# Performance work log

Measured on AMD Instinct MI355X. Metric: run time of the kernel, lower is better.

The kernel has to match this reference:

```python
import jax, jax.numpy as jnp
import numpy as np

B, HORIZON, F, ORDER, K = 8192, 64, 64, 16, 256


def setup_inputs() -> dict:
    key = jax.random.key(0)
    ks = jax.random.split(key, 7)
    s = 0.05
    x = jax.random.normal(ks[0], (B, HORIZON, F), dtype=jnp.float32)
    y0 = jax.random.normal(ks[1], (B, ORDER), dtype=jnp.float32)
    kernel = jax.random.normal(ks[2], (F + ORDER, 4 * K), dtype=jnp.float32) * s
    rec_kernel = jax.random.normal(ks[3], (K, 4 * K), dtype=jnp.float32) * s
    bias = jax.random.normal(ks[4], (4 * K,), dtype=jnp.float32) * s
    dense_w = jax.random.normal(ks[5], (K, 1), dtype=jnp.float32) * s
    dense_b = jax.random.normal(ks[6], (1,), dtype=jnp.float32) * s
    return {"x": x, "y0": y0, "kernel": kernel, "rec_kernel": rec_kernel,
            "bias": bias, "dense_w": dense_w, "dense_b": dense_b}


def reference(x, y0, kernel, rec_kernel, bias, dense_w, dense_b):
    Bn = x.shape[0]
    Ku = rec_kernel.shape[0]
    h0 = jnp.zeros((Bn, Ku), x.dtype)
    c0 = jnp.zeros((Bn, Ku), x.dtype)

    def step(carry, x_t):
        h, c, yp = carry  # yp: [B, order], newest prediction first
        inp = jnp.concatenate([x_t, yp], axis=1)          # [B, F+order]
        z = inp @ kernel + h @ rec_kernel + bias          # [B, 4K]
        i, f, g, o = jnp.split(z, 4, axis=1)              # Keras gate order i,f,c,o
        i = jax.nn.sigmoid(i)
        f = jax.nn.sigmoid(f)
        g = jnp.tanh(g)
        o = jax.nn.sigmoid(o)
        c_new = f * c + i * g
        h_new = o * jnp.tanh(c_new)
        pred = h_new @ dense_w + dense_b                  # [B, 1]
        # tf.roll(shift=1)[:, 1:] then concat([pred, .]) == shift-in newest pred
        yp_new = jnp.concatenate([pred, yp[:, :-1]], axis=1)
        return (h_new, c_new, yp_new), pred

    xs = jnp.transpose(x, (1, 0, 2))                      # [horizon, B, F]
    _, preds = jax.lax.scan(step, (h0, c0, y0), xs)       # preds: [horizon, B, 1]
    return jnp.transpose(preds, (1, 0, 2))                # [B, horizon, 1]
```

## Files before the change

### kernel.cpp

```cpp
#include <hip/hip_runtime.h>
#include <stdint.h>


typedef short v8s __attribute__((ext_vector_type(8)));
typedef float v4f __attribute__((ext_vector_type(4)));

#define NKS 11
#define NKCOL 1024

__device__ __forceinline__ unsigned bf16u(float f) {
  unsigned u = __float_as_uint(f);
  return (u + 0x7FFFu + ((u >> 16) & 1u)) >> 16;
}
__device__ __forceinline__ float sigm(float x) {
  return __builtin_amdgcn_rcpf(1.f + __expf(-x));
}
__device__ __forceinline__ float tanh_(float x) {
  return 1.f - 2.f * __builtin_amdgcn_rcpf(1.f + __expf(2.f * x));
}
__device__ __forceinline__ int a_addr(int m, int k) {
  return (((m >> 4) * NKS + (k >> 5)) << 10)
       + ((((k >> 3) & 3) * 16 + (m & 15)) << 4)
       + ((k & 7) << 1);
}

__global__ void prep_w(const float* __restrict__ ker, const float* __restrict__ rec,
                       uint4* __restrict__ wsw) {
  int tid = blockIdx.x * 256 + threadIdx.x;
  int lane = tid & 63;
  int rest = tid >> 6;
  int ks = rest % NKS;
  int nt = rest / NKS;
  int n  = nt * 16 + (lane & 15);
  int k0 = ks * 32 + ((lane >> 4) & 3) * 8;
  unsigned h[8];
  #pragma unroll
  for (int j = 0; j < 8; ++j) {
    int k = k0 + j;
    float v = 0.f;
    if (k < 80)       v = ker[k * NKCOL + n];
    else if (k < 336) v = rec[(k - 80) * NKCOL + n];
    h[j] = bf16u(v);
  }
  uint4 o;
  o.x = h[0] | (h[1] << 16); o.y = h[2] | (h[3] << 16);
  o.z = h[4] | (h[5] << 16); o.w = h[6] | (h[7] << 16);
  wsw[tid] = o;
}

__global__ __launch_bounds__(512, 2)
void lstm_main(const float* __restrict__ x, const float* __restrict__ y0,
               const float* __restrict__ bias, const float* __restrict__ dw,
               const float* __restrict__ db, const v8s* __restrict__ wv,
               float* __restrict__ out) {
  __shared__ __align__(16) char a_lds[2 * NKS * 1024];
  __shared__ float predbuf[32][8];
  __shared__ float predf[32];

  const int tid  = threadIdx.x;
  const int lane = tid & 63;
  const int wave = tid >> 6;
  const int l15  = lane & 15;
  const int quad = lane >> 4;
  const int b0   = blockIdx.x * 32;

  for (int i = tid; i < 2 * NKS * 256; i += 512) ((unsigned*)a_lds)[i] = 0;

  float bias_v[8];
  int wb[8];
  #pragma unroll
  for (int ln = 0; ln < 8; ++ln) {
    int g = ln >> 1, s = ln & 1;
    int ntg = g * 16 + wave * 2 + s;
    wb[ln] = ntg * NKS * 64;
    bias_v[ln] = bias[ntg * 16 + l15];
  }
  float dw_v[2];
  dw_v[0] = dw[wave * 32 + l15];
  dw_v[1] = dw[wave * 32 + 16 + l15];
  const float dbv = db[0];

  float cst[2][2][4];
  #pragma unroll
  for (int mt = 0; mt < 2; ++mt)
    #pragma unroll
    for (int s = 0; s < 2; ++s)
      #pragma unroll
      for (int r = 0; r < 4; ++r) cst[mt][s][r] = 0.f;

  __syncthreads();

  #pragma unroll 1
  for (int t = 0; t < 64; ++t) {
    unsigned xw[4];
    unsigned short q0 = 0, q1 = 0;
    float pin = 0.f;
    int ms, kq8, jj;
    if (tid < 256) {
      ms = tid >> 3; kq8 = tid & 7;
      const float* xp = x + ((size_t)((b0 + ms) * 64 + t)) * 64 + kq8 * 8;
      float4 xa = ((const float4*)xp)[0];
      float4 xb = ((const float4*)xp)[1];
      xw[0] = bf16u(xa.x) | (bf16u(xa.y) << 16);
      xw[1] = bf16u(xa.z) | (bf16u(xa.w) << 16);
      xw[2] = bf16u(xb.x) | (bf16u(xb.y) << 16);
      xw[3] = bf16u(xb.z) | (bf16u(xb.w) << 16);
    } else {
      int idx = tid - 256; ms = idx >> 3; jj = idx & 7;
      if (t == 0) {
        q0 = (unsigned short)bf16u(y0[(b0 + ms) * 16 + 2 * jj]);
        q1 = (unsigned short)bf16u(y0[(b0 + ms) * 16 + 2 * jj + 1]);
      } else {
        q0 = *(const unsigned short*)(a_lds + a_addr(ms, 64 + 2 * jj));
        q1 = *(const unsigned short*)(a_lds + a_addr(ms, 64 + 2 * jj + 1));
        pin = predf[ms];
      }
    }
    __syncthreads();
    if (tid < 256) {
      uint4 w4; w4.x = xw[0]; w4.y = xw[1]; w4.z = xw[2]; w4.w = xw[3];
      *(uint4*)(a_lds + a_addr(ms, kq8 * 8)) = w4;
    } else {
      if (t == 0) {
        *(unsigned short*)(a_lds + a_addr(ms, 64 + 2 * jj))     = q0;
        *(unsigned short*)(a_lds + a_addr(ms, 64 + 2 * jj + 1)) = q1;
      } else {
        if (jj < 7) {
          *(unsigned short*)(a_lds + a_addr(ms, 64 + 2 * jj + 1)) = q0;
          *(unsigned short*)(a_lds + a_addr(ms, 64 + 2 * jj + 2)) = q1;
        } else {
          *(unsigned short*)(a_lds + a_addr(ms, 79)) = q0;
        }
        if (jj == 0)
          *(unsigned short*)(a_lds + a_addr(ms, 64)) = (unsigned short)bf16u(pin);
      }
    }
    __syncthreads();

    v4f acc[2][8];
    #pragma unroll
    for (int mt = 0; mt < 2; ++mt)
      #pragma unroll
      for (int ln = 0; ln < 8; ++ln) acc[mt][ln] = v4f{0.f, 0.f, 0.f, 0.f};

    v8s bl[8], af0, af1;
    #pragma unroll
    for (int ln = 0; ln < 8; ++ln) bl[ln] = wv[wb[ln] + lane];
    af0 = *(const v8s*)(a_lds + (lane << 4));
    af1 = *(const v8s*)(a_lds + (NKS << 10) + (lane << 4));
    #pragma unroll
    for (int ks = 0; ks < NKS; ++ks) {
      v8s bc[8];
      #pragma unroll
      for (int ln = 0; ln < 8; ++ln) bc[ln] = bl[ln];
      v8s c0 = af0, c1 = af1;
      if (ks < NKS - 1) {
        #pragma unroll
        for (int ln = 0; ln < 8; ++ln) bl[ln] = wv[wb[ln] + (ks + 1) * 64 + lane];
        af0 = *(const v8s*)(a_lds + ((ks + 1) << 10) + (lane << 4));
        af1 = *(const v8s*)(a_lds + ((NKS + ks + 1) << 10) + (lane << 4));
      }
      #pragma unroll
      for (int ln = 0; ln < 8; ++ln) {
        acc[0][ln] = __builtin_amdgcn_mfma_f32_16x16x32_bf16(c0, bc[ln], acc[0][ln], 0, 0, 0);
        acc[1][ln] = __builtin_amdgcn_mfma_f32_16x16x32_bf16(c1, bc[ln], acc[1][ln], 0, 0, 0);
      }
    }
    __syncthreads();

    float padd[2][4];
    #pragma unroll
    for (int mt = 0; mt < 2; ++mt)
      #pragma unroll
      for (int r = 0; r < 4; ++r) padd[mt][r] = 0.f;

    #pragma unroll
    for (int mt = 0; mt < 2; ++mt) {
      #pragma unroll
      for (int s = 0; s < 2; ++s) {
        const int kk = 80 + wave * 32 + s * 16 + l15;
        #pragma unroll
        for (int r = 0; r < 4; ++r) {
          float zi = acc[mt][0 + s][r] + bias_v[0 + s];
          float zf = acc[mt][2 + s][r] + bias_v[2 + s];
          float zg = acc[mt][4 + s][r] + bias_v[4 + s];
          float zo = acc[mt][6 + s][r] + bias_v[6 + s];
          float is = sigm(zi), fs = sigm(zf), gs = tanh_(zg), os = sigm(zo);
          float cn = fs * cst[mt][s][r] + is * gs;
          cst[mt][s][r] = cn;
          float hh = os * tanh_(cn);
          int m = mt * 16 + quad * 4 + r;
          *(unsigned short*)(a_lds + a_addr(m, kk)) = (unsigned short)bf16u(hh);
          padd[mt][r] += hh * dw_v[s];
        }
      }
    }
    #pragma unroll
    for (int mt = 0; mt < 2; ++mt) {
      #pragma unroll
      for (int r = 0; r < 4; ++r) {
        float p = padd[mt][r];
        p += __shfl_xor(p, 1);
        p += __shfl_xor(p, 2);
        p += __shfl_xor(p, 4);
        p += __shfl_xor(p, 8);
        if (l15 == 0) predbuf[mt * 16 + quad * 4 + r][wave] = p;
      }
    }
    __syncthreads();
    if (tid < 32) {
      float p = dbv;
      #pragma unroll
      for (int w = 0; w < 8; ++w) p += predbuf[tid][w];
      out[(size_t)(b0 + tid) * 64 + t] = p;
      predf[tid] = p;
    }
    __syncthreads();
  }
}

extern "C" void kernel_launch(void* const* d_in, const int* in_sizes, int n_in,
                              void* d_out, int out_size, void* d_ws, size_t ws_size,
                              hipStream_t stream) {
  const float* x    = (const float*)d_in[0];
  const float* y0   = (const float*)d_in[1];
  const float* ker  = (const float*)d_in[2];
  const float* rec  = (const float*)d_in[3];
  const float* bias = (const float*)d_in[4];
  const float* dw   = (const float*)d_in[5];
  const float* db   = (const float*)d_in[6];

  prep_w<<<dim3(176), dim3(256), 0, stream>>>(ker, rec, (uint4*)d_ws);
  lstm_main<<<dim3(256), dim3(512), 0, stream>>>(x, y0, bias, dw, db,
                                                 (const v8s*)d_ws, (float*)d_out);
}
```

Before: 1.527 ms.

## Cache early weight k-slices in registers and LDS, prefetch next x

Keeps the first two k-slices of the bf16 weight tiles resident in registers and the next two in a 128KB LDS buffer. Only the remaining seven slices are streamed from global memory each timestep. Also prefetches the next timestep's x row during the gate math, and issues the first streamed weight loads before the barrier. This cuts repeated L2/global weight traffic on the serial recurrence, but adds substantial register pressure under the 512x2 launch bound, which risks spills. The 128KB of LDS limits each CU to one block.

```diff
diff --git a/kernel.cpp b/kernel.cpp
--- a/kernel.cpp
+++ b/kernel.cpp
@@ -54,20 +54,21 @@
                const float* __restrict__ db, const v8s* __restrict__ wv,
                float* __restrict__ out) {
   __shared__ __align__(16) char a_lds[2 * NKS * 1024];
+  __shared__ __align__(16) char w_lds[131072];
   __shared__ float predbuf[32][8];
   __shared__ float predf[32];
 
   const int tid  = threadIdx.x;
   const int lane = tid & 63;
-  const int wave = tid >> 6;
+  const int wave = __builtin_amdgcn_readfirstlane(tid >> 6);
   const int l15  = lane & 15;
   const int quad = lane >> 4;
   const int b0   = blockIdx.x * 32;
 
   for (int i = tid; i < 2 * NKS * 256; i += 512) ((unsigned*)a_lds)[i] = 0;
 
+  int wb[8];
   float bias_v[8];
-  int wb[8];
   #pragma unroll
   for (int ln = 0; ln < 8; ++ln) {
     int g = ln >> 1, s = ln & 1;
@@ -75,11 +76,24 @@
     wb[ln] = ntg * NKS * 64;
     bias_v[ln] = bias[ntg * 16 + l15];
   }
-  float dw_v[2];
-  dw_v[0] = dw[wave * 32 + l15];
-  dw_v[1] = dw[wave * 32 + 16 + l15];
+  float dw_v0 = dw[wave * 32 + l15];
+  float dw_v1 = dw[wave * 32 + 16 + l15];
   const float dbv = db[0];
 
+  v8s wreg[2][8];
+  #pragma unroll
+  for (int ks = 0; ks < 2; ++ks)
+    #pragma unroll
+    for (int ln = 0; ln < 8; ++ln)
+      wreg[ks][ln] = wv[wb[ln] + ks * 64 + lane];
+
+  char* wl = w_lds + wave * 16384 + (lane << 4);
+  #pragma unroll
+  for (int ks = 0; ks < 2; ++ks)
+    #pragma unroll
+    for (int ln = 0; ln < 8; ++ln)
+      *(v8s*)(wl + ks * 8192 + ln * 1024) = wv[wb[ln] + (2 + ks) * 64 + lane];
+
   float cst[2][2][4];
   #pragma unroll
   for (int mt = 0; mt < 2; ++mt)
@@ -87,52 +101,60 @@
     for (int s = 0; s < 2; ++s)
       #pragma unroll
       for (int r = 0; r < 4; ++r) cst[mt][s][r] = 0.f;
+
+  const int ms_x = tid >> 3;
+  const int kq8  = tid & 7;
+  const int ms_y = (tid - 256) >> 3;
+  const int jj   = (tid - 256) & 7;
+
+  float4 xpa, xpb;
+  if (tid < 256) {
+    const float* xp = x + ((size_t)((b0 + ms_x) * 64 + 0)) * 64 + kq8 * 8;
+    xpa = ((const float4*)xp)[0];
+    xpb = ((const float4*)xp)[1];
+  }
 
   __syncthreads();
 
   #pragma unroll 1
   for (int t = 0; t < 64; ++t) {
-    unsigned xw[4];
+    v8s bl[8];
+    #pragma unroll
+    for (int ln = 0; ln < 8; ++ln) bl[ln] = wv[wb[ln] + 4 * 64 + lane];
+
     unsigned short q0 = 0, q1 = 0;
     float pin = 0.f;
-    int ms, kq8, jj;
+    if (tid >= 256) {
+      if (t == 0) {
+        q0 = (unsigned short)bf16u(y0[(b0 + ms_y) * 16 + 2 * jj]);
+        q1 = (unsigned short)bf16u(y0[(b0 + ms_y) * 16 + 2 * jj + 1]);
+      } else {
+        q0 = *(const unsigned short*)(a_lds + a_addr(ms_y, 64 + 2 * jj));
+        q1 = *(const unsigned short*)(a_lds + a_addr(ms_y, 64 + 2 * jj + 1));
+        pin = predf[ms_y];
+      }
+    }
+    __syncthreads();
     if (tid < 256) {
-      ms = tid >> 3; kq8 = tid & 7;
-      const float* xp = x + ((size_t)((b0 + ms) * 64 + t)) * 64 + kq8 * 8;
-      float4 xa = ((const float4*)xp)[0];
-      float4 xb = ((const float4*)xp)[1];
-      xw[0] = bf16u(xa.x) | (bf16u(xa.y) << 16);
-      xw[1] = bf16u(xa.z) | (bf16u(xa.w) << 16);
-      xw[2] = bf16u(xb.x) | (bf16u(xb.y) << 16);
-      xw[3] = bf16u(xb.z) | (bf16u(xb.w) << 16);
-    } else {
-      int idx = tid - 256; ms = idx >> 3; jj = idx & 7;
-      if (t == 0) {
-        q0 = (unsigned short)bf16u(y0[(b0 + ms) * 16 + 2 * jj]);
-        q1 = (unsigned short)bf16u(y0[(b0 + ms) * 16 + 2 * jj + 1]);
-      } else {
-        q0 = *(const unsigned short*)(a_lds + a_addr(ms, 64 + 2 * jj));
-        q1 = *(const unsigned short*)(a_lds + a_addr(ms, 64 + 2 * jj + 1));
-        pin = predf[ms];
-      }
-    }
-    __syncthreads();
-    if (tid < 256) {
-      uint4 w4; w4.x = xw[0]; w4.y = xw[1]; w4.z = xw[2]; w4.w = xw[3];
-      *(uint4*)(a_lds + a_addr(ms, kq8 * 8)) = w4;
+      uint4 w4;
+      w4.x = bf16u(xpa.x) | (bf16u(xpa.y) << 16);
+      w4.y = bf16u(xpa.z) | (bf16u(xpa.w) << 16);
+      w4.z = bf16u(xpb.x) | (bf16u(xpb.y) << 16);
+      w4.w = bf16u(xpb.z) | (bf16u(xpb.w) << 16);
+      *(uint4*)(a_lds + a_addr(ms_x, kq8 * 8)) = w4;
     } else {
       if (t == 0) {
-        *(unsigned short*)(a_lds + a_addr(ms, 64 + 2 * jj))     = q0;
-        *(unsigned short*)(a_lds + a_addr(ms, 64 + 2 * jj + 1)) = q1;
+        *(unsigned short*)(a_lds + a_addr(ms_y, 64 + 2 * jj))     = q0;
+        *(unsigned short*)(a_lds + a_addr(ms_y, 64 + 2 * jj + 1)) = q1;
       } else {
         if (jj < 7) {
-          *(unsigned short*)(a_lds + a_addr(ms, 64 + 2 * jj + 1)) = q0;
-          *(unsigned short*)(a_lds + a_addr(ms, 64 + 2 * jj + 2)) = q1;
+          *(unsigned short*)(a_lds + a_addr(ms_y, 64 + 2 * jj + 1)) = q0;
+          *(unsigned short*)(a_lds + a_addr(ms_y, 64 + 2 * jj + 2)) = q1;
         } else {
-          *(unsigned short*)(a_lds + a_addr(ms, 79)) = q0;
+          *(unsigned short*)(a_lds + a_addr(ms_y, 79)) = q0;
         }
         if (jj == 0)
-          *(unsigned short*)(a_lds + a_addr(ms, 64)) = (unsigned short)bf16u(pin);
+          *(unsigned short*)(a_lds + a_addr(ms_y, 64)) = (unsigned short)bf16u(pin);
       }
     }
     __syncthreads();
@@ -143,30 +165,51 @@
       #pragma unroll
       for (int ln = 0; ln < 8; ++ln) acc[mt][ln] = v4f{0.f, 0.f, 0.f, 0.f};
 
-    v8s bl[8], af0, af1;
-    #pragma unroll
-    for (int ln = 0; ln < 8; ++ln) bl[ln] = wv[wb[ln] + lane];
-    af0 = *(const v8s*)(a_lds + (lane << 4));
-    af1 = *(const v8s*)(a_lds + (NKS << 10) + (lane << 4));
-    #pragma unroll
-    for (int ks = 0; ks < NKS; ++ks) {
-      v8s bc[8];
-      #pragma unroll
-      for (int ln = 0; ln < 8; ++ln) bc[ln] = bl[ln];
-      v8s c0 = af0, c1 = af1;
+    #pragma unroll
+    for (int ks = 0; ks < 2; ++ks) {
+      v8s a0 = *(const v8s*)(a_lds + (ks << 10) + (lane << 4));
+      v8s a1 = *(const v8s*)(a_lds + ((NKS + ks) << 10) + (lane << 4));
+      #pragma unroll
+      for (int ln = 0; ln < 8; ++ln) {
+        acc[0][ln] = __builtin_amdgcn_mfma_f32_16x16x32_bf16(a0, wreg[ks][ln], acc[0][ln], 0, 0, 0);
+        acc[1][ln] = __builtin_amdgcn_mfma_f32_16x16x32_bf16(a1, wreg[ks][ln], acc[1][ln], 0, 0, 0);
+      }
+    }
+    #pragma unroll
+    for (int ks = 2; ks < 4; ++ks) {
+      v8s a0 = *(const v8s*)(a_lds + (ks << 10) + (lane << 4));
+      v8s a1 = *(const v8s*)(a_lds + ((NKS + ks) << 10) + (lane << 4));
+      #pragma unroll
+      for (int ln = 0; ln < 8; ++ln) {
+        v8s bw = *(const v8s*)(wl + (ks - 2) * 8192 + ln * 1024);
+        acc[0][ln] = __builtin_amdgcn_mfma_f32_16x16x32_bf16(a0, bw, acc[0][ln], 0, 0, 0);
+        acc[1][ln] = __builtin_amdgcn_mfma_f32_16x16x32_bf16(a1, bw, acc[1][ln], 0, 0, 0);
+      }
+    }
+    #pragma unroll
+    for (int ks = 4; ks < NKS; ++ks) {
+      v8s a0 = *(const v8s*)(a_lds + (ks << 10) + (lane << 4));
+      v8s a1 = *(const v8s*)(a_lds + ((NKS + ks) << 10) + (lane << 4));
+      v8s cur[8];
+      #pragma unroll
+      for (int ln = 0; ln < 8; ++ln) cur[ln] = bl[ln];
       if (ks < NKS - 1) {
         #pragma unroll
         for (int ln = 0; ln < 8; ++ln) bl[ln] = wv[wb[ln] + (ks + 1) * 64 + lane];
-        af0 = *(const v8s*)(a_lds + ((ks + 1) << 10) + (lane << 4));
-        af1 = *(const v8s*)(a_lds + ((NKS + ks + 1) << 10) + (lane << 4));
       }
       #pragma unroll
       for (int ln = 0; ln < 8; ++ln) {
-        acc[0][ln] = __builtin_amdgcn_mfma_f32_16x16x32_bf16(c0, bc[ln], acc[0][ln], 0, 0, 0);
-        acc[1][ln] = __builtin_amdgcn_mfma_f32_16x16x32_bf16(c1, bc[ln], acc[1][ln], 0, 0, 0);
-      }
-    }
-    __syncthreads();
+        acc[0][ln] = __builtin_amdgcn_mfma_f32_16x16x32_bf16(a0, cur[ln], acc[0][ln], 0, 0, 0);
+        acc[1][ln] = __builtin_amdgcn_mfma_f32_16x16x32_bf16(a1, cur[ln], acc[1][ln], 0, 0, 0);
+      }
+    }
+    __syncthreads();
+
+    if (tid < 256 && t < 63) {
+      const float* xp = x + ((size_t)((b0 + ms_x) * 64 + t + 1)) * 64 + kq8 * 8;
+      xpa = ((const float4*)xp)[0];
+      xpb = ((const float4*)xp)[1];
+    }
 
     float padd[2][4];
     #pragma unroll
@@ -191,7 +234,8 @@
           float hh = os * tanh_(cn);
           int m = mt * 16 + quad * 4 + r;
           *(unsigned short*)(a_lds + a_addr(m, kk)) = (unsigned short)bf16u(hh);
-          padd[mt][r] += hh * dw_v[s];
+          float dwv = (s == 0) ? dw_v0 : dw_v1;
+          padd[mt][r] += hh * dwv;
         }
       }
     }
```

New measurement: 1.532 ms. Within noise of the previous version (+0.3%).

## Split hidden units across block pairs with resident weights and flag-synced exchange

Applied to the files above, without the earlier changes.

Each batch tile of 64 rows is now handled by two cooperating blocks, each owning half of the hidden units. Each block keeps its weight slice resident in registers and LDS instead of re-reading it from global memory every timestep. Partner blocks exchange their new hidden states and partial predictions through workspace slots, synchronised with per-block atomic flags and spin-waits. This removes the repeated weight streaming, but adds inter-block global-memory traffic and depends on all 256 blocks being co-resident, or the spin-waits can deadlock.

```diff
diff --git a/kernel.cpp b/kernel.cpp
--- a/kernel.cpp
+++ b/kernel.cpp
@@ -6,7 +6,10 @@
 typedef float v4f __attribute__((ext_vector_type(4)));
 
 #define NKS 11
-#define NKCOL 1024
+#define WS_FLAGS    720896u
+#define WS_SLOTS    (1u << 20)
+#define SLOT_STRIDE 16896u
+#define SLOT_PRED   16384u
 
 __device__ __forceinline__ unsigned bf16u(float f) {
   unsigned u = __float_as_uint(f);
@@ -25,197 +28,262 @@
 }
 
 __global__ void prep_w(const float* __restrict__ ker, const float* __restrict__ rec,
-                       uint4* __restrict__ wsw) {
+                       char* __restrict__ ws) {
   int tid = blockIdx.x * 256 + threadIdx.x;
-  int lane = tid & 63;
-  int rest = tid >> 6;
-  int ks = rest % NKS;
-  int nt = rest / NKS;
-  int n  = nt * 16 + (lane & 15);
-  int k0 = ks * 32 + ((lane >> 4) & 3) * 8;
-  unsigned h[8];
-  #pragma unroll
-  for (int j = 0; j < 8; ++j) {
-    int k = k0 + j;
-    float v = 0.f;
-    if (k < 80)       v = ker[k * NKCOL + n];
-    else if (k < 336) v = rec[(k - 80) * NKCOL + n];
-    h[j] = bf16u(v);
-  }
-  uint4 o;
-  o.x = h[0] | (h[1] << 16); o.y = h[2] | (h[3] << 16);
-  o.z = h[4] | (h[5] << 16); o.w = h[6] | (h[7] << 16);
-  wsw[tid] = o;
+  if (tid < 45056) {
+    uint4* wsw = (uint4*)ws;
+    int lane = tid & 63;
+    int rest = tid >> 6;
+    int ks = rest % NKS;
+    int nt = rest / NKS;
+    int n  = nt * 16 + (lane & 15);
+    int k0 = ks * 32 + ((lane >> 4) & 3) * 8;
+    unsigned h[8];
+    #pragma unroll
+    for (int j = 0; j < 8; ++j) {
+      int k = k0 + j;
+      float v = 0.f;
+      if (k < 80)       v = ker[k * 1024 + n];
+      else if (k < 336) v = rec[(k - 80) * 1024 + n];
+      h[j] = bf16u(v);
+    }
+    uint4 o;
+    o.x = h[0] | (h[1] << 16); o.y = h[2] | (h[3] << 16);
+    o.z = h[4] | (h[5] << 16); o.w = h[6] | (h[7] << 16);
+    wsw[tid] = o;
+  } else if (tid < 45312) {
+    ((unsigned*)(ws + WS_FLAGS))[tid - 45056] = 0u;
+  }
 }
 
 __global__ __launch_bounds__(512, 2)
 void lstm_main(const float* __restrict__ x, const float* __restrict__ y0,
                const float* __restrict__ bias, const float* __restrict__ dw,
                const float* __restrict__ db, const v8s* __restrict__ wv,
-               float* __restrict__ out) {
-  __shared__ __align__(16) char a_lds[2 * NKS * 1024];
-  __shared__ float predbuf[32][8];
-  __shared__ float predf[32];
+               char* __restrict__ ws, float* __restrict__ out) {
+  __shared__ __align__(16) char a_lds[NKS * 4 * 1024];
+  __shared__ __align__(16) char w_lds[98304];
+  __shared__ float predbuf[64][8];
+  __shared__ float predmine[64];
+  __shared__ float predf2[64];
 
   const int tid  = threadIdx.x;
   const int lane = tid & 63;
-  const int wave = tid >> 6;
+  const int wave = __builtin_amdgcn_readfirstlane(tid >> 6);
   const int l15  = lane & 15;
   const int quad = lane >> 4;
-  const int b0   = blockIdx.x * 32;
-
-  for (int i = tid; i < 2 * NKS * 256; i += 512) ((unsigned*)a_lds)[i] = 0;
-
-  float bias_v[8];
-  int wb[8];
+  const int bid  = blockIdx.x;
+  const int hf   = bid >> 7;
+  const int p    = bid & 127;
+  const int partner = bid ^ 128;
+  const int b0   = p * 64;
+
+  unsigned* flags = (unsigned*)(ws + WS_FLAGS);
+
+  for (int i = tid; i < NKS * 4 * 256; i += 512) ((unsigned*)a_lds)[i] = 0;
+
+  int wb[4];
+  float bias_v[4];
   #pragma unroll
-  for (int ln = 0; ln < 8; ++ln) {
-    int g = ln >> 1, s = ln & 1;
-    int ntg = g * 16 + wave * 2 + s;
-    wb[ln] = ntg * NKS * 64;
-    bias_v[ln] = bias[ntg * 16 + l15];
-  }
-  float dw_v[2];
-  dw_v[0] = dw[wave * 32 + l15];
-  dw_v[1] = dw[wave * 32 + 16 + l15];
+  for (int g = 0; g < 4; ++g) {
+    int nt = g * 16 + hf * 8 + wave;
+    wb[g] = nt * (NKS * 64);
+    bias_v[g] = bias[nt * 16 + l15];
+  }
+  const int u_loc  = wave * 16 + l15;
+  const int u_glob = hf * 128 + u_loc;
+  const int kk = 80 + u_glob;
+  const float dwv = dw[u_glob];
   const float dbv = db[0];
 
-  float cst[2][2][4];
+  v8s wreg[8][4];
   #pragma unroll
-  for (int mt = 0; mt < 2; ++mt)
-    #pragma unroll
-    for (int s = 0; s < 2; ++s)
-      #pragma unroll
-      for (int r = 0; r < 4; ++r) cst[mt][s][r] = 0.f;
+  for (int ks = 0; ks < 8; ++ks)
+    #pragma unroll
+    for (int g = 0; g < 4; ++g)
+      wreg[ks][g] = wv[wb[g] + ks * 64 + lane];
+
+  {
+    char* wlp = w_lds + wave * 12288 + (lane << 4);
+    #pragma unroll
+    for (int ks2 = 0; ks2 < 3; ++ks2)
+      #pragma unroll
+      for (int g = 0; g < 4; ++g)
+        *(v8s*)(wlp + ks2 * 4096 + g * 1024) = wv[wb[g] + (8 + ks2) * 64 + lane];
+  }
+
+  float cst[4][4];
+  #pragma unroll
+  for (int mt = 0; mt < 4; ++mt)
+    #pragma unroll
+    for (int r = 0; r < 4; ++r) cst[mt][r] = 0.f;
+
+  const int ms = tid >> 3;
+  const int jj = tid & 7;
 
   __syncthreads();
 
   #pragma unroll 1
   for (int t = 0; t < 64; ++t) {
-    unsigned xw[4];
-    unsigned short q0 = 0, q1 = 0;
-    float pin = 0.f;
-    int ms, kq8, jj;
-    if (tid < 256) {
-      ms = tid >> 3; kq8 = tid & 7;
-      const float* xp = x + ((size_t)((b0 + ms) * 64 + t)) * 64 + kq8 * 8;
+    if (t > 0) {
+      if (tid == 0) {
+        unsigned* pf = flags + partner;
+        while (__hip_atomic_load(pf, __ATOMIC_RELAXED, __HIP_MEMORY_SCOPE_AGENT) < (unsigned)t)
+          __builtin_amdgcn_s_sleep(2);
+      }
+      __syncthreads();
+      __threadfence();
+    }
+    {
+      const float* xp = x + (((size_t)(b0 + ms) * 64 + t) << 6) + (jj << 3);
       float4 xa = ((const float4*)xp)[0];
       float4 xb = ((const float4*)xp)[1];
-      xw[0] = bf16u(xa.x) | (bf16u(xa.y) << 16);
-      xw[1] = bf16u(xa.z) | (bf16u(xa.w) << 16);
-      xw[2] = bf16u(xb.x) | (bf16u(xb.y) << 16);
-      xw[3] = bf16u(xb.z) | (bf16u(xb.w) << 16);
+      uint4 w4;
+      w4.x = bf16u(xa.x) | (bf16u(xa.y) << 16);
+      w4.y = bf16u(xa.z) | (bf16u(xa.w) << 16);
+      w4.z = bf16u(xb.x) | (bf16u(xb.y) << 16);
+      w4.w = bf16u(xb.z) | (bf16u(xb.w) << 16);
+      *(uint4*)(a_lds + a_addr(ms, jj * 8)) = w4;
+    }
+    unsigned short q0, q1;
+    if (t == 0) {
+      q0 = (unsigned short)bf16u(y0[(b0 + ms) * 16 + 2 * jj]);
+      q1 = (unsigned short)bf16u(y0[(b0 + ms) * 16 + 2 * jj + 1]);
     } else {
-      int idx = tid - 256; ms = idx >> 3; jj = idx & 7;
-      if (t == 0) {
-        q0 = (unsigned short)bf16u(y0[(b0 + ms) * 16 + 2 * jj]);
-        q1 = (unsigned short)bf16u(y0[(b0 + ms) * 16 + 2 * jj + 1]);
+      q0 = *(const unsigned short*)(a_lds + a_addr(ms, 64 + 2 * jj));
+      q1 = *(const unsigned short*)(a_lds + a_addr(ms, 64 + 2 * jj + 1));
+      const char* pslot = ws + WS_SLOTS
+          + (size_t)(((p * 2 + (1 - hf)) * 2) + ((t - 1) & 1)) * SLOT_STRIDE;
+      uint4 h0 = *(const uint4*)(pslot + ms * 256 + (jj << 5));
+      uint4 h1 = *(const uint4*)(pslot + ms * 256 + (jj << 5) + 16);
+      int k0 = 80 + (1 - hf) * 128 + (jj << 4);
+      *(uint4*)(a_lds + a_addr(ms, k0)) = h0;
+      *(uint4*)(a_lds + a_addr(ms, k0 + 8)) = h1;
+      if (tid < 64) {
+        float pp = predmine[tid] + *(const float*)(pslot + SLOT_PRED + (tid << 2)) + dbv;
+        predf2[tid] = pp;
+        if (hf == 0) out[((size_t)(b0 + tid) << 6) + (t - 1)] = pp;
+      }
+    }
+    __syncthreads();
+    if (t == 0) {
+      *(unsigned short*)(a_lds + a_addr(ms, 64 + 2 * jj))     = q0;
+      *(unsigned short*)(a_lds + a_addr(ms, 64 + 2 * jj + 1)) = q1;
+    } else {
+      if (jj < 7) {
+        *(unsigned short*)(a_lds + a_addr(ms, 64 + 2 * jj + 1)) = q0;
+        *(unsigned short*)(a_lds + a_addr(ms, 64 + 2 * jj + 2)) = q1;
       } else {
-        q0 = *(const unsigned short*)(a_lds + a_addr(ms, 64 + 2 * jj));
-        q1 = *(const unsigned short*)(a_lds + a_addr(ms, 64 + 2 * jj + 1));
-        pin = predf[ms];
-      }
-    }
-    __syncthreads();
-    if (tid < 256) {
-      uint4 w4; w4.x = xw[0]; w4.y = xw[1]; w4.z = xw[2]; w4.w = xw[3];
-      *(uint4*)(a_lds + a_addr(ms, kq8 * 8)) = w4;
-    } else {
-      if (t == 0) {
-        *(unsigned short*)(a_lds + a_addr(ms, 64 + 2 * jj))     = q0;
-        *(unsigned short*)(a_lds + a_addr(ms, 64 + 2 * jj + 1)) = q1;
-      } else {
-        if (jj < 7) {
-          *(unsigned short*)(a_lds + a_addr(ms, 64 + 2 * jj + 1)) = q0;
-          *(unsigned short*)(a_lds + a_addr(ms, 64 + 2 * jj + 2)) = q1;
-        } else {
-          *(unsigned short*)(a_lds + a_addr(ms, 79)) = q0;
-        }
-        if (jj == 0)
-          *(unsigned short*)(a_lds + a_addr(ms, 64)) = (unsigned short)bf16u(pin);
-      }
-    }
-    __syncthreads();
-
-    v4f acc[2][8];
-    #pragma unroll
-    for (int mt = 0; mt < 2; ++mt)
-      #pragma unroll
-      for (int ln = 0; ln < 8; ++ln) acc[mt][ln] = v4f{0.f, 0.f, 0.f, 0.f};
-
-    v8s bl[8], af0, af1;
-    #pragma unroll
-    for (int ln = 0; ln < 8; ++ln) bl[ln] = wv[wb[ln] + lane];
-    af0 = *(const v8s*)(a_lds + (lane << 4));
-    af1 = *(const v8s*)(a_lds + (NKS << 10) + (lane << 4));
-    #pragma unroll
-    for (int ks = 0; ks < NKS; ++ks) {
-      v8s bc[8];
-      #pragma unroll
-      for (int ln = 0; ln < 8; ++ln) bc[ln] = bl[ln];
-      v8s c0 = af0, c1 = af1;
-      if (ks < NKS - 1) {
-        #pragma unroll
-        for (int ln = 0; ln < 8; ++ln) bl[ln] = wv[wb[ln] + (ks + 1) * 64 + lane];
-        af0 = *(const v8s*)(a_lds + ((ks + 1) << 10) + (lane << 4));
-        af1 = *(const v8s*)(a_lds + ((NKS + ks + 1) << 10) + (lane << 4));
-      }
-      #pragma unroll
-      for (int ln = 0; ln < 8; ++ln) {
-        acc[0][ln] = __builtin_amdgcn_mfma_f32_16x16x32_bf16(c0, bc[ln], acc[0][ln], 0, 0, 0);
-        acc[1][ln] = __builtin_amdgcn_mfma_f32_16x16x32_bf16(c1, bc[ln], acc[1][ln], 0, 0, 0);
-      }
-    }
-    __syncthreads();
-
-    float padd[2][4];
-    #pragma unroll
-    for (int mt = 0; mt < 2; ++mt)
-      #pragma unroll
-      for (int r = 0; r < 4; ++r) padd[mt][r] = 0.f;
-
-    #pragma unroll
-    for (int mt = 0; mt < 2; ++mt) {
-      #pragma unroll
-      for (int s = 0; s < 2; ++s) {
-        const int kk = 80 + wave * 32 + s * 16 + l15;
-        #pragma unroll
-        for (int r = 0; r < 4; ++r) {
-          float zi = acc[mt][0 + s][r] + bias_v[0 + s];
-          float zf = acc[mt][2 + s][r] + bias_v[2 + s];
-          float zg = acc[mt][4 + s][r] + bias_v[4 + s];
-          float zo = acc[mt][6 + s][r] + bias_v[6 + s];
-          float is = sigm(zi), fs = sigm(zf), gs = tanh_(zg), os = sigm(zo);
-          float cn = fs * cst[mt][s][r] + is * gs;
-          cst[mt][s][r] = cn;
-          float hh = os * tanh_(cn);
-          int m = mt * 16 + quad * 4 + r;
-          *(unsigned short*)(a_lds + a_addr(m, kk)) = (unsigned short)bf16u(hh);
-          padd[mt][r] += hh * dw_v[s];
-        }
-      }
-    }
-    #pragma unroll
-    for (int mt = 0; mt < 2; ++mt) {
+        *(unsigned short*)(a_lds + a_addr(ms, 79)) = q0;
+      }
+      if (jj == 0)
+        *(unsigned short*)(a_lds + a_addr(ms, 64)) = (unsigned short)bf16u(predf2[ms]);
+    }
+    __syncthreads();
+
+    v4f acc[4][4];
+    #pragma unroll
+    for (int mt = 0; mt < 4; ++mt)
+      #pragma unroll
+      for (int g = 0; g < 4; ++g) acc[mt][g] = v4f{0.f, 0.f, 0.f, 0.f};
+
+    #pragma unroll
+    for (int ks = 0; ks < 8; ++ks) {
+      v8s a0 = *(const v8s*)(a_lds + ((0 * NKS + ks) << 10) + (lane << 4));
+      v8s a1 = *(const v8s*)(a_lds + ((1 * NKS + ks) << 10) + (lane << 4));
+      v8s a2 = *(const v8s*)(a_lds + ((2 * NKS + ks) << 10) + (lane << 4));
+      v8s a3 = *(const v8s*)(a_lds + ((3 * NKS + ks) << 10) + (lane << 4));
+      #pragma unroll
+      for (int g = 0; g < 4; ++g) {
+        acc[0][g] = __builtin_amdgcn_mfma_f32_16x16x32_bf16(a0, wreg[ks][g], acc[0][g], 0, 0, 0);
+        acc[1][g] = __builtin_amdgcn_mfma_f32_16x16x32_bf16(a1, wreg[ks][g], acc[1][g], 0, 0, 0);
+        acc[2][g] = __builtin_amdgcn_mfma_f32_16x16x32_bf16(a2, wreg[ks][g], acc[2][g], 0, 0, 0);
+        acc[3][g] = __builtin_amdgcn_mfma_f32_16x16x32_bf16(a3, wreg[ks][g], acc[3][g], 0, 0, 0);
+      }
+    }
+    #pragma unroll
+    for (int ks2 = 0; ks2 < 3; ++ks2) {
+      const int ks = 8 + ks2;
+      v8s a0 = *(const v8s*)(a_lds + ((0 * NKS + ks) << 10) + (lane << 4));
+      v8s a1 = *(const v8s*)(a_lds + ((1 * NKS + ks) << 10) + (lane << 4));
+      v8s a2 = *(const v8s*)(a_lds + ((2 * NKS + ks) << 10) + (lane << 4));
+      v8s a3 = *(const v8s*)(a_lds + ((3 * NKS + ks) << 10) + (lane << 4));
+      v8s bw[4];
+      #pragma unroll
+      for (int g = 0; g < 4; ++g)
+        bw[g] = *(const v8s*)(w_lds + wave * 12288 + ks2 * 4096 + g * 1024 + (lane << 4));
+      #pragma unroll
+      for (int g = 0; g < 4; ++g) {
+        acc[0][g] = __builtin_amdgcn_mfma_f32_16x16x32_bf16(a0, bw[g], acc[0][g], 0, 0, 0);
+        acc[1][g] = __builtin_amdgcn_mfma_f32_16x16x32_bf16(a1, bw[g], acc[1][g], 0, 0, 0);
+        acc[2][g] = __builtin_amdgcn_mfma_f32_16x16x32_bf16(a2, bw[g], acc[2][g], 0, 0, 0);
+        acc[3][g] = __builtin_amdgcn_mfma_f32_16x16x32_bf16(a3, bw[g], acc[3][g], 0, 0, 0);
+      }
+    }
+    __syncthreads();
+
+    char* myslot = ws + WS_SLOTS + (size_t)(((p * 2 + hf) * 2) + (t & 1)) * SLOT_STRIDE;
+    float padd[4][4];
+    #pragma unroll
+    for (int mt = 0; mt < 4; ++mt) {
       #pragma unroll
       for (int r = 0; r < 4; ++r) {
-        float p = padd[mt][r];
-        p += __shfl_xor(p, 1);
-        p += __shfl_xor(p, 2);
-        p += __shfl_xor(p, 4);
-        p += __shfl_xor(p, 8);
-        if (l15 == 0) predbuf[mt * 16 + quad * 4 + r][wave] = p;
-      }
-    }
-    __syncthreads();
-    if (tid < 32) {
-      float p = dbv;
-      #pragma unroll
-      for (int w = 0; w < 8; ++w) p += predbuf[tid][w];
-      out[(size_t)(b0 + tid) * 64 + t] = p;
-      predf[tid] = p;
-    }
-    __syncthreads();
+        float zi = acc[mt][0][r] + bias_v[0];
+        float zf = acc[mt][1][r] + bias_v[1];
+        float zg = acc[mt][2][r] + bias_v[2];
+        float zo = acc[mt][3][r] + bias_v[3];
+        float is = sigm(zi), fs = sigm(zf), gs = tanh_(zg), os = sigm(zo);
+        float cn = fs * cst[mt][r] + is * gs;
+        cst[mt][r] = cn;
+        float hh = os * tanh_(cn);
+        int m = mt * 16 + quad * 4 + r;
+        unsigned short hb = (unsigned short)bf16u(hh);
+        *(unsigned short*)(a_lds + a_addr(m, kk)) = hb;
+        *(unsigned short*)(myslot + m * 256 + (u_loc << 1)) = hb;
+        padd[mt][r] = hh * dwv;
+      }
+    }
+    #pragma unroll
+    for (int mt = 0; mt < 4; ++mt) {
+      #pragma unroll
+      for (int r = 0; r < 4; ++r) {
+        float pv = padd[mt][r];
+        pv += __shfl_xor(pv, 1);
+        pv += __shfl_xor(pv, 2);
+        pv += __shfl_xor(pv, 4);
+        pv += __shfl_xor(pv, 8);
+        if (l15 == 0) predbuf[mt * 16 + quad * 4 + r][wave] = pv;
+      }
+    }
+    __threadfence();
+    __syncthreads();
+    if (tid < 64) {
+      float s = 0.f;
+      #pragma unroll
+      for (int w = 0; w < 8; ++w) s += predbuf[tid][w];
+      predmine[tid] = s;
+      *(float*)(myslot + SLOT_PRED + (tid << 2)) = s;
+      __threadfence();
+    }
+    __syncthreads();
+    if (tid == 0)
+      __hip_atomic_store(flags + bid, (unsigned)(t + 1),
+                         __ATOMIC_RELEASE, __HIP_MEMORY_SCOPE_AGENT);
+  }
+
+  if (hf == 0) {
+    if (tid == 0) {
+      unsigned* pf = flags + partner;
+      while (__hip_atomic_load(pf, __ATOMIC_RELAXED, __HIP_MEMORY_SCOPE_AGENT) < 64u)
+        __builtin_amdgcn_s_sleep(2);
+    }
+    __syncthreads();
+    __threadfence();
+    if (tid < 64) {
+      const char* pslot = ws + WS_SLOTS + (size_t)(((p * 2 + 1) * 2) + 1) * SLOT_STRIDE;
+      float pp = predmine[tid] + *(const float*)(pslot + SLOT_PRED + (tid << 2)) + dbv;
+      out[((size_t)(b0 + tid) << 6) + 63] = pp;
+    }
   }
 }
 
@@ -230,7 +298,8 @@
   const float* dw   = (const float*)d_in[5];
   const float* db   = (const float*)d_in[6];
 
-  prep_w<<<dim3(176), dim3(256), 0, stream>>>(ker, rec, (uint4*)d_ws);
+  prep_w<<<dim3(177), dim3(256), 0, stream>>>(ker, rec, (char*)d_ws);
   lstm_main<<<dim3(256), dim3(512), 0, stream>>>(x, y0, bias, dw, db,
-                                                 (const v8s*)d_ws, (float*)d_out);
-}
+                                                 (const v8s*)d_ws, (char*)d_ws,
+                                                 (float*)d_out);
+}
```

Result: slower. 5.456 ms (+257.3%).
